# Kernel optimization log

Hardware: AMD Instinct MI355X
Metric: run time of the kernel (lower is better)

Reference implementation:

```python
import jax, jax.numpy as jnp
import numpy as np

DIM = 1536
DEPTH = 8
HEADS = 8
KV_HEADS = 1
GROUPS = HEADS // KV_HEADS
DQK = 128
DV = 192
DIM_PW = 128
POOL = 16
FF_INNER = int(DIM * 2.0)
SOFTCLAMP = 5.0
SCALE = 64 ** -0.5  # source uses default dim_head=64 for scale, not dim_head_qk
MAX_POS = 8192
EPS = float(jnp.finfo(jnp.float32).eps)


def rmsnorm(x, g):
    return x * jax.lax.rsqrt(jnp.mean(x * x, axis=-1, keepdims=True) + EPS) * g


def rotate_half(x):
    x1, x2 = jnp.split(x, 2, axis=-1)
    return jnp.concatenate([-x2, x1], axis=-1)


def apply_rope(pos, t):
    return t * jnp.cos(pos) + rotate_half(t) * jnp.sin(pos)


def rotary_emb(seq_len):
    nf = DQK // 2
    # torch.logspace(1, MAX_POS-nf+1, nf) = 10**linspace -> overflows to inf in fp32 (faithful)
    inv_freq = 1.0 / (jnp.arange(nf, dtype=jnp.float32) + 10.0 ** jnp.linspace(1.0, MAX_POS - nf + 1, nf, dtype=jnp.float32))
    freqs = jnp.arange(seq_len, dtype=jnp.float32)[:, None] * inv_freq[None, :]
    return jnp.concatenate([freqs, freqs], axis=-1)  # [n, DQK]


def softclamp(t, value=SOFTCLAMP):
    return jnp.tanh(t / value) * value


def attention(x, pairwise, rope, w_qkv, qg, kg, vg, bg, w_bias, w_out):
    b, n, _ = x.shape
    qkv = x @ w_qkv
    q, k, v = jnp.split(qkv, [HEADS * DQK, HEADS * DQK + DQK], axis=-1)
    # b n (g h d) -> b g h n d
    q = q.reshape(b, n, GROUPS, KV_HEADS, DQK).transpose(0, 2, 3, 1, 4)
    k = k.reshape(b, n, KV_HEADS, DQK).transpose(0, 2, 1, 3)
    v = v.reshape(b, n, KV_HEADS, DV).transpose(0, 2, 1, 3)
    q = rmsnorm(q, qg)
    k = rmsnorm(k, kg)
    v = rmsnorm(v, vg)
    q = q * SCALE
    q = apply_rope(rope, q)
    k = apply_rope(rope, k)
    sim = jnp.einsum('bghid,bhjd->bghij', q, k)
    # pairwise bias: RMSNorm -> GELU -> Linear(dim_pw, heads) -> b g h i j
    pb = jax.nn.gelu(rmsnorm(pairwise, bg), approximate=False) @ w_bias  # [b, i, j, heads]
    bi = pb.shape[1]
    bias = pb.reshape(b, bi, bi, GROUPS, KV_HEADS).transpose(0, 3, 4, 1, 2)
    bias = jnp.repeat(jnp.repeat(bias, POOL, axis=3), POOL, axis=4)  # expand to seq res
    sim = softclamp(sim + bias)
    attn = jax.nn.softmax(sim, axis=-1)
    out = jnp.einsum('bghij,bhjd->bghid', attn, v)
    out = out.transpose(0, 3, 1, 2, 4).reshape(b, n, GROUPS * KV_HEADS * DV)
    return out @ w_out


def tower(x, pairwise, w_qkv, q_gamma, k_gamma, v_gamma, bias_gamma, w_bias, w_out, attn_pre_gamma, ff_pre_gamma, w_ff1, b_ff1, w_ff2, b_ff2):
    rope = rotary_emb(x.shape[1])
    for d in range(DEPTH):
        xn = rmsnorm(x, attn_pre_gamma[d])
        x = x + attention(xn, pairwise, rope, w_qkv[d], q_gamma[d], k_gamma[d], v_gamma[d], bias_gamma[d], w_bias[d], w_out[d])
        xn = rmsnorm(x, ff_pre_gamma[d])
        x = x + (jax.nn.relu(xn @ w_ff1[d] + b_ff1[d]) @ w_ff2[d] + b_ff2[d])
    return x


def setup_inputs() -> dict:
    key = jax.random.key(0)
    ks = jax.random.split(key, 10)
    s = 0.02
    inp = {
        'x': jax.random.normal(ks[0], (2, 2048, DIM), jnp.float32),
        'pairwise': jax.random.normal(ks[1], (2, 128, 128, DIM_PW), jnp.float32),
        'w_qkv': jax.random.normal(ks[2], (DEPTH, DIM, HEADS * DQK + DQK + DV), jnp.float32) * s,
        'q_gamma': jnp.ones((DEPTH, DQK), jnp.float32),
        'k_gamma': jnp.ones((DEPTH, DQK), jnp.float32),
        'v_gamma': jnp.ones((DEPTH, DV), jnp.float32),
        'bias_gamma': jnp.ones((DEPTH, DIM_PW), jnp.float32),
        'w_bias': jax.random.normal(ks[3], (DEPTH, DIM_PW, HEADS), jnp.float32) * s,
        'w_out': jax.random.normal(ks[4], (DEPTH, DV * HEADS, DIM), jnp.float32) * s,
        'attn_pre_gamma': jnp.ones((DEPTH, DIM), jnp.float32),
        'ff_pre_gamma': jnp.ones((DEPTH, DIM), jnp.float32),
        'w_ff1': jax.random.normal(ks[5], (DEPTH, DIM, FF_INNER), jnp.float32) * s,
        'b_ff1': jnp.zeros((DEPTH, FF_INNER), jnp.float32),
        'w_ff2': jax.random.normal(ks[6], (DEPTH, FF_INNER, DIM), jnp.float32) * s,
        'b_ff2': jnp.zeros((DEPTH, DIM), jnp.float32),
    }
    return inp


def reference(x, pairwise, w_qkv, q_gamma, k_gamma, v_gamma, bias_gamma, w_bias, w_out, attn_pre_gamma, ff_pre_gamma, w_ff1, b_ff1, w_ff2, b_ff2):
    return tower(x, pairwise, w_qkv, q_gamma, k_gamma, v_gamma, bias_gamma, w_bias, w_out, attn_pre_gamma, ff_pre_gamma, w_ff1, b_ff1, w_ff2, b_ff2)
```

## Files before the change

kernel.cpp:

```cpp
#include <hip/hip_runtime.h>

typedef __bf16 bf16;
typedef float f32x4 __attribute__((ext_vector_type(4)));
typedef __bf16 bf16x8 __attribute__((ext_vector_type(8)));
typedef __bf16 bf16x4 __attribute__((ext_vector_type(4)));

#define EPSF 1.1920928955078125e-07f

#define GLOAD_LDS16(gsrc, ldst) \
  __builtin_amdgcn_global_load_lds((const __attribute__((address_space(1))) void*)(gsrc), \
                                   (__attribute__((address_space(3))) void*)(ldst), 16, 0, 0)

__device__ __forceinline__ float wave_reduce_sum(float v) {
#pragma unroll
  for (int m = 1; m < 64; m <<= 1) v += __shfl_xor(v, m, 64);
  return v;
}

__global__ __launch_bounds__(256) void wcast_t(const float* __restrict__ src,
                                               bf16* __restrict__ dst, int R, int C) {
  __shared__ float t[32][33];
  int z = blockIdx.z;
  const float* s = src + (size_t)z * R * C;
  bf16* d = dst + (size_t)z * R * C;
  int c0 = blockIdx.x * 32, r0 = blockIdx.y * 32;
  int tx = threadIdx.x, ty = threadIdx.y;
#pragma unroll
  for (int k = 0; k < 4; ++k)
    t[ty + k * 8][tx] = s[(size_t)(r0 + ty + k * 8) * C + c0 + tx];
  __syncthreads();
#pragma unroll
  for (int k = 0; k < 4; ++k)
    d[(size_t)(c0 + ty + k * 8) * R + r0 + tx] = (bf16)t[tx][ty + k * 8];
}

__global__ __launch_bounds__(256) void rmsnorm_k(const float* __restrict__ X,
                                                 const float* __restrict__ G,
                                                 bf16* __restrict__ O) {
  int row = blockIdx.x, tid = threadIdx.x, lane = tid & 63, w = tid >> 6;
  const float* x = X + (size_t)row * 1536;
  float v[6];
  float ss = 0.f;
#pragma unroll
  for (int k = 0; k < 6; ++k) { v[k] = x[tid + k * 256]; ss += v[k] * v[k]; }
  ss = wave_reduce_sum(ss);
  __shared__ float wsum[4];
  if (lane == 0) wsum[w] = ss;
  __syncthreads();
  ss = wsum[0] + wsum[1] + wsum[2] + wsum[3];
  float rs = rsqrtf(ss * (1.f / 1536.f) + EPSF);
  bf16* o = O + (size_t)row * 1536;
#pragma unroll
  for (int k = 0; k < 6; ++k) o[tid + k * 256] = (bf16)(v[k] * rs * G[tid + k * 256]);
}

template <int EPI>
__global__ __launch_bounds__(256, 3) void gemm_bt(const bf16* __restrict__ A,
                                                  const bf16* __restrict__ Bt,
                                                  float* __restrict__ Cf,
                                                  bf16* __restrict__ Cb,
                                                  const float* __restrict__ bias,
                                                  int M, int N, int K) {
  __shared__ __align__(16) char As[128 * 128];
  __shared__ __align__(16) char Bs[128 * 128];
  const int tid = threadIdx.x;
  const int lane = tid & 63, l15 = lane & 15, l4 = lane >> 4;
  const int w = tid >> 6;
  const int rm = blockIdx.y * 128;
  const int cn = blockIdx.x * 128;
  const int wm = (w >> 1) * 64, wn = (w & 1) * 64;
  f32x4 acc[4][4] = {};

  for (int kk = 0; kk < K; kk += 64) {
#pragma unroll
    for (int r = 0; r < 4; ++r) {
      uint32_t o = (uint32_t)(r * 256 + tid) * 16;
      uint32_t row = o >> 7;
      uint32_t kb = ((o >> 4) & 7) ^ (row & 7);
      const bf16* src = A + (size_t)(rm + (int)row) * K + kk + kb * 8;
      GLOAD_LDS16(src, As + (o & 0xFFFFFC00u));
    }
#pragma unroll
    for (int r = 0; r < 4; ++r) {
      uint32_t o = (uint32_t)(r * 256 + tid) * 16;
      uint32_t row = o >> 7;
      uint32_t kb = ((o >> 4) & 7) ^ (row & 7);
      int nrow = cn + (int)row;
      if (nrow >= N) nrow = N - 1;
      const bf16* src = Bt + (size_t)nrow * K + kk + kb * 8;
      GLOAD_LDS16(src, Bs + (o & 0xFFFFFC00u));
    }
    __syncthreads();
#pragma unroll
    for (int s = 0; s < 2; ++s) {
      bf16x8 a[4], b[4];
#pragma unroll
      for (int m = 0; m < 4; ++m) {
        uint32_t row = wm + m * 16 + l15;
        uint32_t kb = (uint32_t)(s * 4 + l4);
        a[m] = *(const bf16x8*)(As + row * 128 + (kb ^ (row & 7)) * 16);
      }
#pragma unroll
      for (int n = 0; n < 4; ++n) {
        uint32_t row = wn + n * 16 + l15;
        uint32_t kb = (uint32_t)(s * 4 + l4);
        b[n] = *(const bf16x8*)(Bs + row * 128 + (kb ^ (row & 7)) * 16);
      }
      __builtin_amdgcn_s_setprio(1);
#pragma unroll
      for (int m = 0; m < 4; ++m)
#pragma unroll
        for (int n = 0; n < 4; ++n)
          acc[m][n] = __builtin_amdgcn_mfma_f32_16x16x32_bf16(a[m], b[n], acc[m][n], 0, 0, 0);
      __builtin_amdgcn_s_setprio(0);
    }
    __syncthreads();
  }

#pragma unroll
  for (int m = 0; m < 4; ++m)
#pragma unroll
    for (int n = 0; n < 4; ++n)
#pragma unroll
      for (int r = 0; r < 4; ++r) {
        int row = rm + wm + m * 16 + l4 * 4 + r;
        int col = cn + wn + n * 16 + l15;
        if (col < N) {
          float v = acc[m][n][r];
          if constexpr (EPI == 0) {
            Cf[(size_t)row * N + col] = v;
          } else if constexpr (EPI == 2) {
            Cf[(size_t)row * N + col] += v;
          } else if constexpr (EPI == 3) {
            float tv = v + bias[col];
            Cb[(size_t)row * N + col] = (bf16)(tv > 0.f ? tv : 0.f);
          } else if constexpr (EPI == 4) {
            Cf[(size_t)row * N + col] += v + bias[col];
          }
        }
      }
}

__global__ void qkv_post(const float* __restrict__ qkv, const float* __restrict__ qg,
                         const float* __restrict__ kg, const float* __restrict__ vg,
                         bf16* __restrict__ Qo, bf16* __restrict__ Ko, bf16* __restrict__ Vo) {
  int t = blockIdx.x, seg = blockIdx.y, lane = threadIdx.x;
  int b = t >> 11, n = t & 2047;
  const float* base;
  const float* gamma;
  int len;
  if (seg < 8) { base = qkv + (size_t)t * 1344 + seg * 128; gamma = qg; len = 128; }
  else if (seg == 8) { base = qkv + (size_t)t * 1344 + 1024; gamma = kg; len = 128; }
  else { base = qkv + (size_t)t * 1344 + 1152; gamma = vg; len = 192; }
  float v0 = base[lane], v1 = base[lane + 64];
  float v2 = (len == 192) ? base[lane + 128] : 0.f;
  float ss = wave_reduce_sum(v0 * v0 + v1 * v1 + v2 * v2);
  float rs = rsqrtf(ss / (float)len + EPSF);
  float n0 = v0 * rs * gamma[lane];
  float n1 = v1 * rs * gamma[lane + 64];
  if (seg < 8) {
    n0 *= 0.125f; n1 *= 0.125f;
    if (lane == 0) {
      float th = 0.1f * (float)n;
      float c = cosf(th), s_ = sinf(th);
      float r0 = n0 * c - n1 * s_, r1 = n1 * c + n0 * s_;
      n0 = r0; n1 = r1;
    }
    bf16* q = Qo + ((size_t)((b * 8 + seg) * 2048 + n)) * 128;
    q[lane] = (bf16)n0; q[lane + 64] = (bf16)n1;
  } else if (seg == 8) {
    if (lane == 0) {
      float th = 0.1f * (float)n;
      float c = cosf(th), s_ = sinf(th);
      float r0 = n0 * c - n1 * s_, r1 = n1 * c + n0 * s_;
      n0 = r0; n1 = r1;
    }
    bf16* k = Ko + ((size_t)(b * 2048 + n)) * 128;
    k[lane] = (bf16)n0; k[lane + 64] = (bf16)n1;
  } else {
    float n2 = v2 * rs * vg[lane + 128];
    bf16* vp = Vo + ((size_t)(b * 2048 + n)) * 192;
    vp[lane] = (bf16)n0; vp[lane + 64] = (bf16)n1; vp[lane + 128] = (bf16)n2;
  }
}

__global__ __launch_bounds__(256) void vtrans(const bf16* __restrict__ V, bf16* __restrict__ Vt) {
  __shared__ bf16 t[32][33];
  int b = blockIdx.z;
  int j0 = blockIdx.x * 32, d0 = blockIdx.y * 32;
  int tx = threadIdx.x, ty = threadIdx.y;
#pragma unroll
  for (int k = 0; k < 4; ++k)
    t[ty + k * 8][tx] = V[((size_t)b * 2048 + j0 + ty + k * 8) * 192 + d0 + tx];
  __syncthreads();
#pragma unroll
  for (int k = 0; k < 4; ++k)
    Vt[((size_t)b * 192 + d0 + ty + k * 8) * 2048 + j0 + tx] = t[tx][ty + k * 8];
}

__global__ void bias_pw(const float* __restrict__ P, const float* __restrict__ g,
                        const float* __restrict__ Wb, float* __restrict__ Bout) {
  int j = blockIdx.x, i = blockIdx.y, b = blockIdx.z;
  int lane = threadIdx.x;
  const float* p = P + (((size_t)b * 128 + i) * 128 + j) * 128;
  float a0 = p[lane], a1 = p[lane + 64];
  float ss = wave_reduce_sum(a0 * a0 + a1 * a1);
  float rs = rsqrtf(ss * (1.f / 128.f) + EPSF);
  float x0 = a0 * rs * g[lane], x1 = a1 * rs * g[lane + 64];
  float g0 = 0.5f * x0 * (1.f + erff(x0 * 0.70710678118654752f));
  float g1 = 0.5f * x1 * (1.f + erff(x1 * 0.70710678118654752f));
  __shared__ float gs[128];
  gs[lane] = g0; gs[lane + 64] = g1;
  __syncthreads();
  int h = lane & 7;
  float acc = 0.f;
#pragma unroll
  for (int k = 0; k < 16; ++k) {
    int c = (lane >> 3) + k * 8;
    acc += gs[c] * Wb[c * 8 + h];
  }
  acc += __shfl_xor(acc, 8, 64);
  acc += __shfl_xor(acc, 16, 64);
  acc += __shfl_xor(acc, 32, 64);
  if (lane < 8) Bout[(((size_t)b * 8 + lane) * 128 + i) * 128 + j] = acc;
}

__global__ __launch_bounds__(256, 2) void attn_k(const bf16* __restrict__ Q,
                                                 const bf16* __restrict__ Kg,
                                                 const bf16* __restrict__ Vt,
                                                 const float* __restrict__ Bias,
                                                 bf16* __restrict__ O0, bf16* __restrict__ O1,
                                                 float* __restrict__ L0, float* __restrict__ L1) {
  __shared__ __align__(16) char Ks[64 * 256];
  __shared__ __align__(16) char Vs[192 * 128];
  __shared__ __align__(16) char Ps[128 * 128];
  __shared__ float BiasS[8 * 128];
  int tid = threadIdx.x, lane = tid & 63, w = tid >> 6;
  int it = blockIdx.x, g = blockIdx.y, bz = blockIdx.z;
  int b = bz >> 1, js = bz & 1;
  bf16* __restrict__ Op = js ? O1 : O0;
  float* __restrict__ Lp = js ? L1 : L0;
  int i0 = it * 128;
  int l15 = lane & 15, l4 = lane >> 4;

  bf16x8 qf[2][4];
#pragma unroll
  for (int m = 0; m < 2; ++m)
#pragma unroll
    for (int s = 0; s < 4; ++s)
      qf[m][s] = *(const bf16x8*)(Q + ((size_t)((b * 8 + g) * 2048 + i0 + w * 32 + m * 16 + l15)) * 128 + s * 32 + l4 * 8);

  {
    int r = tid >> 5, c = (tid & 31) * 4;
    *(float4*)&BiasS[r * 128 + c] =
        *(const float4*)(Bias + ((size_t)((b * 8 + g) * 128) + (i0 >> 4) + r) * 128 + c);
  }

  f32x4 accO[2][12] = {};
  float lacc[2] = {0.f, 0.f};

  for (int jt = js * 16; jt < js * 16 + 16; ++jt) {
    int j0 = jt * 64;
#pragma unroll
    for (int r = 0; r < 4; ++r) {
      uint32_t o = (uint32_t)(r * 256 + tid) * 16;
      uint32_t row = o >> 8;
      uint32_t kb = ((o >> 4) & 15) ^ (row & 15);
      const bf16* src = Kg + ((size_t)b * 2048 + j0 + (int)row) * 128 + kb * 8;
      GLOAD_LDS16(src, Ks + (o & 0xFFFFFC00u));
    }
#pragma unroll
    for (int r = 0; r < 6; ++r) {
      uint32_t o = (uint32_t)(r * 256 + tid) * 16;
      uint32_t dv = o >> 7;
      uint32_t kb = ((o >> 4) & 7) ^ (dv & 7);
      const bf16* src = Vt + ((size_t)b * 192 + dv) * 2048 + j0 + kb * 8;
      GLOAD_LDS16(src, Vs + (o & 0xFFFFFC00u));
    }
    __syncthreads();

    f32x4 accS[2][4] = {};
#pragma unroll
    for (int s = 0; s < 4; ++s) {
      bf16x8 kf[4];
#pragma unroll
      for (int n = 0; n < 4; ++n) {
        uint32_t row = n * 16 + l15;
        uint32_t kb = (uint32_t)(s * 4 + l4);
        kf[n] = *(const bf16x8*)(Ks + row * 256 + (kb ^ (row & 15)) * 16);
      }
      __builtin_amdgcn_s_setprio(1);
#pragma unroll
      for (int n = 0; n < 4; ++n)
#pragma unroll
        for (int m = 0; m < 2; ++m)
          accS[m][n] = __builtin_amdgcn_mfma_f32_16x16x32_bf16(kf[n], qf[m][s], accS[m][n], 0, 0, 0);
      __builtin_amdgcn_s_setprio(0);
    }

#pragma unroll
    for (int m = 0; m < 2; ++m) {
#pragma unroll
      for (int n = 0; n < 4; ++n) {
        float bia = BiasS[(w * 2 + m) * 128 + jt * 4 + n];
        bf16x4 pk;
#pragma unroll
        for (int r = 0; r < 4; ++r) {
          float sv = accS[m][n][r] + bia;
          float e1 = exp2f(0.57707801635558535f * sv);
          float th = 1.f - 2.f / (e1 + 1.f);
          float pv = exp2f(7.2134752044448170f * th);
          lacc[m] += pv;
          pk[r] = (bf16)pv;
        }
        uint32_t prow = (uint32_t)(w * 32 + m * 16 + l15);
        uint32_t byteo = prow * 128 + (uint32_t)(n * 16 + l4 * 4) * 2;
        byteo ^= (prow & 7) << 4;
        *(bf16x4*)(Ps + byteo) = pk;
      }
    }

#pragma unroll
    for (int s = 0; s < 2; ++s) {
      bf16x8 pa[2];
#pragma unroll
      for (int m = 0; m < 2; ++m) {
        uint32_t row = (uint32_t)(w * 32 + m * 16 + l15);
        uint32_t byteo = row * 128 + (uint32_t)(s * 64 + l4 * 16);
        byteo ^= (row & 7) << 4;
        pa[m] = *(const bf16x8*)(Ps + byteo);
      }
#pragma unroll
      for (int n = 0; n < 12; ++n) {
        uint32_t dvr = n * 16 + l15;
        uint32_t kb = (uint32_t)(s * 4 + l4);
        bf16x8 vf = *(const bf16x8*)(Vs + dvr * 128 + (kb ^ (dvr & 7)) * 16);
        __builtin_amdgcn_s_setprio(1);
#pragma unroll
        for (int m = 0; m < 2; ++m)
          accO[m][n] = __builtin_amdgcn_mfma_f32_16x16x32_bf16(vf, pa[m], accO[m][n], 0, 0, 0);
        __builtin_amdgcn_s_setprio(0);
      }
    }
    __syncthreads();
  }

#pragma unroll
  for (int m = 0; m < 2; ++m) {
    float l = lacc[m];
    l += __shfl_xor(l, 16, 64);
    l += __shfl_xor(l, 32, 64);
    lacc[m] = l;
  }
  if (l4 == 0) {
#pragma unroll
    for (int m = 0; m < 2; ++m)
      Lp[(size_t)(b * 8 + g) * 2048 + i0 + w * 32 + m * 16 + l15] = lacc[m];
  }

#pragma unroll
  for (int m = 0; m < 2; ++m) {
    int i = i0 + w * 32 + m * 16 + l15;
#pragma unroll
    for (int n = 0; n < 12; ++n) {
      bf16x4 ok;
#pragma unroll
      for (int r = 0; r < 4; ++r) ok[r] = (bf16)accO[m][n][r];
      int dv = n * 16 + l4 * 4;
      *(bf16x4*)(Op + ((size_t)(b * 8 + g) * 2048 + i) * 192 + dv) = ok;
    }
  }
}

__global__ __launch_bounds__(256) void attn_cmb(const bf16* __restrict__ O0,
                                                const bf16* __restrict__ O1,
                                                const float* __restrict__ L0,
                                                const float* __restrict__ L1,
                                                bf16* __restrict__ Out) {
  size_t e = ((size_t)blockIdx.x * 256u + threadIdx.x) * 8u;
  uint32_t dv = (uint32_t)(e % 192u);
  uint32_t rest = (uint32_t)(e / 192u);
  uint32_t i = rest & 2047u;
  uint32_t g = (rest >> 11) & 7u;
  uint32_t b = rest >> 14;
  bf16x8 a = *(const bf16x8*)(O0 + e);
  bf16x8 c = *(const bf16x8*)(O1 + e);
  float rl = 1.f / (L0[rest] + L1[rest]);
  bf16x8 t;
#pragma unroll
  for (int k = 0; k < 8; ++k) t[k] = (bf16)(((float)a[k] + (float)c[k]) * rl);
  *(bf16x8*)(Out + ((size_t)(b * 2048 + i)) * 1536 + g * 192 + dv) = t;
}

extern "C" void kernel_launch(void* const* d_in, const int* in_sizes, int n_in,
                              void* d_out, int out_size, void* d_ws, size_t ws_size,
                              hipStream_t stream) {
  (void)in_sizes; (void)n_in; (void)out_size;
  const float* x_in = (const float*)d_in[0];
  const float* pairwise = (const float*)d_in[1];
  const float* w_qkv = (const float*)d_in[2];
  const float* q_gamma = (const float*)d_in[3];
  const float* k_gamma = (const float*)d_in[4];
  const float* v_gamma = (const float*)d_in[5];
  const float* bias_gamma = (const float*)d_in[6];
  const float* w_bias = (const float*)d_in[7];
  const float* w_out = (const float*)d_in[8];
  const float* attn_pre = (const float*)d_in[9];
  const float* ff_pre = (const float*)d_in[10];
  const float* w_ff1 = (const float*)d_in[11];
  const float* b_ff1 = (const float*)d_in[12];
  const float* w_ff2 = (const float*)d_in[13];
  const float* b_ff2 = (const float*)d_in[14];

  char* p = (char*)d_ws;
  auto alloc = [&](size_t bytes) {
    char* r = p;
    p += (bytes + 255) & ~(size_t)255;
    return r;
  };
  bf16* wT_qkv = (bf16*)alloc(8ull * 1344 * 1536 * 2);
  bf16* wT_out = (bf16*)alloc(8ull * 1536 * 1536 * 2);
  bf16* wT_ff1 = (bf16*)alloc(8ull * 3072 * 1536 * 2);
  bf16* wT_ff2 = (bf16*)alloc(8ull * 1536 * 3072 * 2);
  float* x_ws = (float*)alloc(4096ull * 1536 * 4);
  bf16* xn = (bf16*)alloc(4096ull * 1536 * 2);
  float* qkvb = (float*)alloc(4096ull * 1344 * 4);
  bf16* qb = (bf16*)alloc(2ull * 8 * 2048 * 128 * 2);
  bf16* kb = (bf16*)alloc(2ull * 2048 * 128 * 2);
  bf16* vb = (bf16*)alloc(2ull * 2048 * 192 * 2);
  bf16* vtb = (bf16*)alloc(2ull * 192 * 2048 * 2);
  float* biasb = (float*)alloc(2ull * 8 * 128 * 128 * 4);
  bf16* attn_o = (bf16*)alloc(4096ull * 1536 * 2);
  bf16* hb = (bf16*)alloc(4096ull * 3072 * 2);
  bf16* op0 = (bf16*)alloc(2ull * 8 * 2048 * 192 * 2);
  bf16* op1 = (bf16*)alloc(2ull * 8 * 2048 * 192 * 2);
  float* lp0 = (float*)alloc(2ull * 8 * 2048 * 4);
  float* lp1 = (float*)alloc(2ull * 8 * 2048 * 4);
  if ((size_t)(p - (char*)d_ws) > ws_size) return;

  wcast_t<<<dim3(42, 48, 8), dim3(32, 8), 0, stream>>>(w_qkv, wT_qkv, 1536, 1344);
  wcast_t<<<dim3(48, 48, 8), dim3(32, 8), 0, stream>>>(w_out, wT_out, 1536, 1536);
  wcast_t<<<dim3(96, 48, 8), dim3(32, 8), 0, stream>>>(w_ff1, wT_ff1, 1536, 3072);
  wcast_t<<<dim3(48, 96, 8), dim3(32, 8), 0, stream>>>(w_ff2, wT_ff2, 3072, 1536);

  hipMemcpyAsync(x_ws, x_in, 4096ull * 1536 * 4, hipMemcpyDeviceToDevice, stream);

  for (int d = 0; d < 8; ++d) {
    const bf16* wq = wT_qkv + (size_t)d * 1344 * 1536;
    const bf16* wo = wT_out + (size_t)d * 1536 * 1536;
    const bf16* w1 = wT_ff1 + (size_t)d * 3072 * 1536;
    const bf16* w2 = wT_ff2 + (size_t)d * 1536 * 3072;

    rmsnorm_k<<<4096, 256, 0, stream>>>(x_ws, attn_pre + d * 1536, xn);
    gemm_bt<0><<<dim3(11, 32), 256, 0, stream>>>(xn, wq, qkvb, nullptr, nullptr, 4096, 1344, 1536);
    qkv_post<<<dim3(4096, 10), 64, 0, stream>>>(qkvb, q_gamma + d * 128, k_gamma + d * 128,
                                                v_gamma + d * 192, qb, kb, vb);
    vtrans<<<dim3(64, 6, 2), dim3(32, 8), 0, stream>>>(vb, vtb);
    bias_pw<<<dim3(128, 128, 2), 64, 0, stream>>>(pairwise, bias_gamma + d * 128,
                                                  w_bias + d * 128 * 8, biasb);
    attn_k<<<dim3(16, 8, 4), 256, 0, stream>>>(qb, kb, vtb, biasb, op0, op1, lp0, lp1);
    attn_cmb<<<3072, 256, 0, stream>>>(op0, op1, lp0, lp1, attn_o);
    gemm_bt<2><<<dim3(12, 32), 256, 0, stream>>>(attn_o, wo, x_ws, nullptr, nullptr, 4096, 1536, 1536);
    rmsnorm_k<<<4096, 256, 0, stream>>>(x_ws, ff_pre + d * 1536, xn);
    gemm_bt<3><<<dim3(24, 32), 256, 0, stream>>>(xn, w1, nullptr, hb, b_ff1 + d * 3072, 4096, 3072, 1536);
    gemm_bt<4><<<dim3(12, 32), 256, 0, stream>>>(hb, w2, x_ws, nullptr, b_ff2 + d * 1536, 4096, 1536, 3072);
  }

  hipMemcpyAsync(d_out, x_ws, 4096ull * 1536 * 4, hipMemcpyDeviceToDevice, stream);
}
```

Baseline: 2.876 ms.

## Double-buffer GEMM LDS tiles and simplify softclamp-softmax exponent math

The GEMM kernel now keeps two LDS buffers and issues the next K-tile's global-to-LDS loads before computing the current tile, so memory latency overlaps MFMA work with one barrier per iteration. Occupancy is lowered from 3 to 2 blocks because LDS use doubles. In attention, the bias is pre-scaled by the tanh constant so the softclamp becomes one FMA, a hardware reciprocal and a folded exp2 constant (the exp(5) factor cancels in normalisation). The combine kernel also uses the fast reciprocal, trading a little precision for fewer instructions.

```diff
diff --git a/kernel.cpp b/kernel.cpp
--- a/kernel.cpp
+++ b/kernel.cpp
@@ -55,14 +55,14 @@
 }
 
 template <int EPI>
-__global__ __launch_bounds__(256, 3) void gemm_bt(const bf16* __restrict__ A,
+__global__ __launch_bounds__(256, 2) void gemm_bt(const bf16* __restrict__ A,
                                                   const bf16* __restrict__ Bt,
                                                   float* __restrict__ Cf,
                                                   bf16* __restrict__ Cb,
                                                   const float* __restrict__ bias,
                                                   int M, int N, int K) {
-  __shared__ __align__(16) char As[128 * 128];
-  __shared__ __align__(16) char Bs[128 * 128];
+  __shared__ __align__(16) char As[2][128 * 64 * 2];
+  __shared__ __align__(16) char Bs[2][128 * 64 * 2];
   const int tid = threadIdx.x;
   const int lane = tid & 63, l15 = lane & 15, l4 = lane >> 4;
   const int w = tid >> 6;
@@ -71,26 +71,22 @@
   const int wm = (w >> 1) * 64, wn = (w & 1) * 64;
   f32x4 acc[4][4] = {};
 
-  for (int kk = 0; kk < K; kk += 64) {
+  auto STAGE = [&](int buf, int kk) {
 #pragma unroll
     for (int r = 0; r < 4; ++r) {
       uint32_t o = (uint32_t)(r * 256 + tid) * 16;
       uint32_t row = o >> 7;
       uint32_t kb = ((o >> 4) & 7) ^ (row & 7);
-      const bf16* src = A + (size_t)(rm + (int)row) * K + kk + kb * 8;
-      GLOAD_LDS16(src, As + (o & 0xFFFFFC00u));
-    }
-#pragma unroll
-    for (int r = 0; r < 4; ++r) {
-      uint32_t o = (uint32_t)(r * 256 + tid) * 16;
-      uint32_t row = o >> 7;
-      uint32_t kb = ((o >> 4) & 7) ^ (row & 7);
+      const bf16* srcA = A + (size_t)(rm + (int)row) * K + kk + kb * 8;
+      GLOAD_LDS16(srcA, &As[buf][0] + (o & 0xFFFFFC00u));
       int nrow = cn + (int)row;
       if (nrow >= N) nrow = N - 1;
-      const bf16* src = Bt + (size_t)nrow * K + kk + kb * 8;
-      GLOAD_LDS16(src, Bs + (o & 0xFFFFFC00u));
-    }
-    __syncthreads();
+      const bf16* srcB = Bt + (size_t)nrow * K + kk + kb * 8;
+      GLOAD_LDS16(srcB, &Bs[buf][0] + (o & 0xFFFFFC00u));
+    }
+  };
+
+  auto COMPUTE = [&](int buf) {
 #pragma unroll
     for (int s = 0; s < 2; ++s) {
       bf16x8 a[4], b[4];
@@ -98,13 +94,13 @@
       for (int m = 0; m < 4; ++m) {
         uint32_t row = wm + m * 16 + l15;
         uint32_t kb = (uint32_t)(s * 4 + l4);
-        a[m] = *(const bf16x8*)(As + row * 128 + (kb ^ (row & 7)) * 16);
+        a[m] = *(const bf16x8*)(&As[buf][0] + row * 128 + (kb ^ (row & 7)) * 16);
       }
 #pragma unroll
       for (int n = 0; n < 4; ++n) {
         uint32_t row = wn + n * 16 + l15;
         uint32_t kb = (uint32_t)(s * 4 + l4);
-        b[n] = *(const bf16x8*)(Bs + row * 128 + (kb ^ (row & 7)) * 16);
+        b[n] = *(const bf16x8*)(&Bs[buf][0] + row * 128 + (kb ^ (row & 7)) * 16);
       }
       __builtin_amdgcn_s_setprio(1);
 #pragma unroll
@@ -114,8 +110,18 @@
           acc[m][n] = __builtin_amdgcn_mfma_f32_16x16x32_bf16(a[m], b[n], acc[m][n], 0, 0, 0);
       __builtin_amdgcn_s_setprio(0);
     }
+  };
+
+  STAGE(0, 0);
+  __syncthreads();
+  int cur = 0;
+  for (int kk = 64; kk < K; kk += 64) {
+    STAGE(cur ^ 1, kk);
+    COMPUTE(cur);
     __syncthreads();
-  }
+    cur ^= 1;
+  }
+  COMPUTE(cur);
 
 #pragma unroll
   for (int m = 0; m < 4; ++m)
@@ -252,8 +258,10 @@
 
   {
     int r = tid >> 5, c = (tid & 31) * 4;
-    *(float4*)&BiasS[r * 128 + c] =
-        *(const float4*)(Bias + ((size_t)((b * 8 + g) * 128) + (i0 >> 4) + r) * 128 + c);
+    float4 bv = *(const float4*)(Bias + ((size_t)((b * 8 + g) * 128) + (i0 >> 4) + r) * 128 + c);
+    bv.x *= 0.57707801635558535f; bv.y *= 0.57707801635558535f;
+    bv.z *= 0.57707801635558535f; bv.w *= 0.57707801635558535f;
+    *(float4*)&BiasS[r * 128 + c] = bv;
   }
 
   f32x4 accO[2][12] = {};
@@ -302,14 +310,14 @@
     for (int m = 0; m < 2; ++m) {
 #pragma unroll
       for (int n = 0; n < 4; ++n) {
-        float bia = BiasS[(w * 2 + m) * 128 + jt * 4 + n];
+        float biaS = BiasS[(w * 2 + m) * 128 + jt * 4 + n];
         bf16x4 pk;
 #pragma unroll
         for (int r = 0; r < 4; ++r) {
-          float sv = accS[m][n][r] + bia;
-          float e1 = exp2f(0.57707801635558535f * sv);
-          float th = 1.f - 2.f / (e1 + 1.f);
-          float pv = exp2f(7.2134752044448170f * th);
+          float t1 = __builtin_fmaf(0.57707801635558535f, accS[m][n][r], biaS);
+          float e1 = exp2f(t1);
+          float rr = __builtin_amdgcn_rcpf(e1 + 1.0f);
+          float pv = exp2f(-14.426950408889634f * rr);
           lacc[m] += pv;
           pk[r] = (bf16)pv;
         }
@@ -385,7 +393,7 @@
   uint32_t b = rest >> 14;
   bf16x8 a = *(const bf16x8*)(O0 + e);
   bf16x8 c = *(const bf16x8*)(O1 + e);
-  float rl = 1.f / (L0[rest] + L1[rest]);
+  float rl = __builtin_amdgcn_rcpf(L0[rest] + L1[rest]);
   bf16x8 t;
 #pragma unroll
   for (int k = 0; k < 8; ++k) t[k] = (bf16)(((float)a[k] + (float)c[k]) * rl);
```

Result: slower. 3.098 ms (+7.7%).
